# Optimization experiments

Hardware: AMD Instinct MI355X
Metric: run time of the kernel (lower is better)

## Reference

```python
import jax, jax.numpy as jnp
import numpy as np

TIMESTEPS = 1000
ZERO_W = 1.0
NONZERO_W = 1.0
VT_W = 1.0
VX_W = 1.0
VY_W = 1.0


def _holographic_transform(x, timesteps, transpose):
    """x: (B,1,H,W) -> (B,1,H,timesteps).
    For each nonzero pixel (h,w) with value v, write w (the column index) at
    time bin q = int(v*timesteps)-1 (negative q wraps, as torch's x[-1]=...).
    Torch iterates nonzeros in row-major order so on collisions the largest
    column index wins -> scatter-max reproduces that deterministically.
    """
    img = x[:, 0]
    if transpose:  # virtual_dim == 'x'
        img = jnp.swapaxes(img, 1, 2)
    B, H, W = img.shape
    q = (img * timesteps).astype(jnp.int32) - 1
    # zeros -> out-of-range index `timesteps`, dropped by mode='drop';
    # nonzeros: wrap -1 -> timesteps-1 like torch negative indexing
    q = jnp.where(img != 0, q % timesteps, timesteps)
    ycoord = jnp.broadcast_to(jnp.arange(W, dtype=x.dtype), (B, H, W))
    b_idx = jnp.arange(B)[:, None, None]
    h_idx = jnp.arange(H)[None, :, None]
    out = jnp.zeros((B, H, timesteps), x.dtype)
    out = out.at[b_idx, h_idx, q].max(ycoord, mode='drop')
    return out[:, None]


def _acb_mse(recon, target, zero_w, nonzero_w):
    zero_mask = target == 0
    d2 = (recon - target) ** 2
    c0 = zero_mask.sum()
    c1 = (~zero_mask).sum()
    # mean over each class; empty class (NaN in torch) -> 0
    l0 = jnp.where(c0 > 0, jnp.where(zero_mask, d2, 0.0).sum() / jnp.maximum(c0, 1), 0.0)
    l1 = jnp.where(c1 > 0, jnp.where(zero_mask, 0.0, d2).sum() / jnp.maximum(c1, 1), 0.0)
    return zero_w * l0 + nonzero_w * l1


def setup_inputs() -> dict:
    key = jax.random.key(0)
    k1, k2, k3, k4 = jax.random.split(key, 4)
    B, H, W = 32, 512, 512

    def sparse_img(kv, km):
        v = jax.random.uniform(kv, (B, 1, H, W), dtype=jnp.float32)
        keep = jax.random.uniform(km, (B, 1, H, W)) < 0.05
        return jnp.where(keep, v, 0.0)

    return {
        "reconstructed_image": sparse_img(k1, k2),
        "target_image": sparse_img(k3, k4),
    }


def reference(reconstructed_image, target_image):
    vt = _acb_mse(reconstructed_image, target_image, ZERO_W, NONZERO_W) * VT_W

    rx = _holographic_transform(reconstructed_image, TIMESTEPS, transpose=True)
    tx = _holographic_transform(target_image, TIMESTEPS, transpose=True)
    vx = _acb_mse(rx, tx, ZERO_W, NONZERO_W) * VX_W

    ry = _holographic_transform(reconstructed_image, TIMESTEPS, transpose=False)
    ty = _holographic_transform(target_image, TIMESTEPS, transpose=False)
    vy = _acb_mse(ry, ty, ZERO_W, NONZERO_W) * VY_W

    return vt + vx + vy
```

## Files before the change

kernel.cpp:

```cpp
#include <hip/hip_runtime.h>

#define TS 1000

__device__ __forceinline__ double wred(double v) {
#pragma unroll
    for (int o = 32; o > 0; o >>= 1) v += __shfl_down(v, o, 64);
    return v;
}

__device__ __forceinline__ void scat(unsigned* bins, float v, unsigned val) {
    if (v != 0.0f) {
        int q = (int)(v * 1000.0f) - 1;
        if (q < 0) q += TS;
        atomicMax(&bins[q], val);
    }
}

__global__ void kinit(double* acc, int n) {
    int i = blockIdx.x * blockDim.x + threadIdx.x;
    if (i < n) acc[i] = 0.0;
}

__global__ __launch_bounds__(256, 4) void kmain(const float* __restrict__ R,
                                                const float* __restrict__ T,
                                                double* __restrict__ acc,
                                                int ncopy_mask) {
    __shared__ unsigned bins[8000];
    const int tid = threadIdx.x;
    const uint4 z4 = make_uint4(0u, 0u, 0u, 0u);

    {
        uint4* p = (uint4*)bins;
        for (int i = tid; i < 2000; i += 256) p[i] = z4;
    }
    __syncthreads();

    const int lane = tid & 63, wv = tid >> 6;
    const int id = blockIdx.x;
    double* accrow = acc + (size_t)(id & ncopy_mask) * 16;

    double s0 = 0.0, ssum = 0.0;
    int c1 = 0;

    if ((id & 1) == 0) {
        const int kid = id >> 1;
        double t0 = 0.0, tsum = 0.0;
        int tc1 = 0;
        unsigned* bR = bins + wv * 2000;
        unsigned* bT = bR + 1000;
        uint4* r4 = (uint4*)bR;
        uint4* t4 = (uint4*)bT;
        for (int it = 0; it < 4; it++) {
            const size_t row = (size_t)kid * 16 + (size_t)(wv * 4 + it);
            const float4* R4 = (const float4*)(R + row * 512);
            const float4* T4 = (const float4*)(T + row * 512);
#pragma unroll
            for (int k = 0; k < 2; k++) {
                const int c = lane + k * 64;
                float4 rv = R4[c];
                float4 tv = T4[c];
                float rr[4] = {rv.x, rv.y, rv.z, rv.w};
                float tt[4] = {tv.x, tv.y, tv.z, tv.w};
#pragma unroll
                for (int j = 0; j < 4; j++) {
                    float a = rr[j], b = tt[j];
                    float d = a - b, d2 = d * d;
                    bool bz = (b == 0.0f);
                    tsum += (double)d2;
                    t0 += bz ? (double)d2 : 0.0;
                    tc1 += bz ? 0 : 1;
                    scat(bR, a, (unsigned)(c * 4 + j));
                    scat(bT, b, (unsigned)(c * 4 + j));
                }
            }
            __syncthreads();
            for (int g = lane; g < 250; g += 64) {
                uint4 rg = r4[g], tg = t4[g];
                if (rg.x | rg.y | rg.z | rg.w | tg.x | tg.y | tg.z | tg.w) {
                    r4[g] = z4;
                    t4[g] = z4;
                    unsigned ru[4] = {rg.x, rg.y, rg.z, rg.w};
                    unsigned tu[4] = {tg.x, tg.y, tg.z, tg.w};
#pragma unroll
                    for (int j2 = 0; j2 < 4; j2++) {
                        float rb = (float)ru[j2], tb = (float)tu[j2];
                        float d = rb - tb, d2 = d * d;
                        bool tz = (tb == 0.0f);
                        ssum += (double)d2;
                        s0 += tz ? (double)d2 : 0.0;
                        c1 += tz ? 0 : 1;
                    }
                }
            }
            __syncthreads();
        }
        double v0 = wred(t0), v1 = wred(tsum), v2 = wred((double)tc1);
        double v3 = wred(s0), v4 = wred(ssum), v5 = wred((double)c1);
        if (lane == 0) {
            atomicAdd(&accrow[0], v0);
            atomicAdd(&accrow[1], v1);
            atomicAdd(&accrow[2], v2);
            atomicAdd(&accrow[3], v3);
            atomicAdd(&accrow[4], v4);
            atomicAdd(&accrow[5], v5);
        }
    } else {
        const int kid = id >> 1;
        const int b = kid >> 5;
        const int line = kid & 31;
        const float* Rb = R + (size_t)b * (512 * 512) + (size_t)line * 16;
        const float* Tb = T + (size_t)b * (512 * 512) + (size_t)line * 16;

        float4 ra[8], ta[8];
#pragma unroll
        for (int k = 0; k < 8; k++) {
            const int h = k * 64 + (tid >> 2);
            const int sub = (tid + k) & 3;
            const size_t off = (size_t)h * 512 + sub * 4;
            ra[k] = *(const float4*)(Rb + off);
            ta[k] = *(const float4*)(Tb + off);
        }

        uint4* r4 = (uint4*)bins;
        uint4* t4 = (uint4*)(bins + 4000);
#pragma unroll
        for (int p = 0; p < 4; p++) {
#pragma unroll
            for (int k = 0; k < 8; k++) {
                if (((tid + k) & 3) == p) {
                    const unsigned h = (unsigned)(k * 64 + (tid >> 2));
                    scat(bins + 0 * 1000, ra[k].x, h);
                    scat(bins + 1 * 1000, ra[k].y, h);
                    scat(bins + 2 * 1000, ra[k].z, h);
                    scat(bins + 3 * 1000, ra[k].w, h);
                    scat(bins + 4000 + 0 * 1000, ta[k].x, h);
                    scat(bins + 4000 + 1 * 1000, ta[k].y, h);
                    scat(bins + 4000 + 2 * 1000, ta[k].z, h);
                    scat(bins + 4000 + 3 * 1000, ta[k].w, h);
                }
            }
            __syncthreads();
            for (int g = tid; g < 1000; g += 256) {
                uint4 rg = r4[g], tg = t4[g];
                if (rg.x | rg.y | rg.z | rg.w | tg.x | tg.y | tg.z | tg.w) {
                    r4[g] = z4;
                    t4[g] = z4;
                    unsigned ru[4] = {rg.x, rg.y, rg.z, rg.w};
                    unsigned tu[4] = {tg.x, tg.y, tg.z, tg.w};
#pragma unroll
                    for (int j = 0; j < 4; j++) {
                        float rb = (float)ru[j], tb = (float)tu[j];
                        float d = rb - tb, d2 = d * d;
                        bool tz = (tb == 0.0f);
                        ssum += (double)d2;
                        s0 += tz ? (double)d2 : 0.0;
                        c1 += tz ? 0 : 1;
                    }
                }
            }
            __syncthreads();
        }
        double v3 = wred(s0), v4 = wred(ssum), v5 = wred((double)c1);
        if (lane == 0) {
            atomicAdd(&accrow[6], v3);
            atomicAdd(&accrow[7], v4);
            atomicAdd(&accrow[8], v5);
        }
    }
}

__global__ void kfin(const double* __restrict__ acc, float* __restrict__ out,
                     int ncopy) {
    const int lane = threadIdx.x;
    double v[9];
#pragma unroll
    for (int k = 0; k < 9; k++) v[k] = 0.0;
    if (lane < ncopy) {
#pragma unroll
        for (int k = 0; k < 9; k++) v[k] = acc[(size_t)lane * 16 + k];
    }
#pragma unroll
    for (int k = 0; k < 9; k++) {
#pragma unroll
        for (int o = 16; o > 0; o >>= 1) v[k] += __shfl_down(v[k], o, 64);
    }
    if (lane == 0) {
        const double NT = 8388608.0;
        const double NB = 16384000.0;
        double vt_c1 = v[2], vy_c1 = v[5], vx_c1 = v[8];
        double vt_c0 = NT - vt_c1, vy_c0 = NB - vy_c1, vx_c0 = NB - vx_c1;
        double vt_s1 = v[1] - v[0];
        double vy_s1 = v[4] - v[3];
        double vx_s1 = v[7] - v[6];
        double vt = (vt_c0 > 0.0 ? v[0] / vt_c0 : 0.0) +
                    (vt_c1 > 0.0 ? vt_s1 / vt_c1 : 0.0);
        double vy = (vy_c0 > 0.0 ? v[3] / vy_c0 : 0.0) +
                    (vy_c1 > 0.0 ? vy_s1 / vy_c1 : 0.0);
        double vx = (vx_c0 > 0.0 ? v[6] / vx_c0 : 0.0) +
                    (vx_c1 > 0.0 ? vx_s1 / vx_c1 : 0.0);
        out[0] = (float)(vt + vx + vy);
    }
}

extern "C" void kernel_launch(void* const* d_in, const int* in_sizes, int n_in,
                              void* d_out, int out_size, void* d_ws, size_t ws_size,
                              hipStream_t stream) {
    const float* R = (const float*)d_in[0];
    const float* T = (const float*)d_in[1];
    double* acc = (double*)d_ws;
    float* out = (float*)d_out;

    int ncopy = 16;
    while (ncopy > 1 && (size_t)ncopy * 16 * sizeof(double) > ws_size) ncopy >>= 1;

    hipLaunchKernelGGL(kinit, dim3(1), dim3(256), 0, stream, acc, ncopy * 16);
    hipLaunchKernelGGL(kmain, dim3(2048), dim3(256), 0, stream, R, T, acc, ncopy - 1);
    hipLaunchKernelGGL(kfin, dim3(1), dim3(64), 0, stream, acc, out, ncopy);
}
```

Baseline: 83.10 us.

## Fuse finalize into main kernel, use float accumulators, raise occupancy bound

Drops the separate init and finalize kernels. A memset now clears the workspace, and a last-block-done atomic counter lets the final block compute the loss inside the main kernel. Per-thread accumulators switch from double to float and are widened to double only for the warp reduction. The launch bound moves from 4 to 5 blocks per CU, and one trailing barrier is removed. The float accumulation slightly reduces precision, and the fused finalize adds a threadfence plus an atomic counter per block.

Result: slower. 146.7 us (+76.5%).

```diff
diff --git a/kernel.cpp b/kernel.cpp
--- a/kernel.cpp
+++ b/kernel.cpp
@@ -16,15 +16,12 @@
     }
 }
 
-__global__ void kinit(double* acc, int n) {
-    int i = blockIdx.x * blockDim.x + threadIdx.x;
-    if (i < n) acc[i] = 0.0;
-}
-
-__global__ __launch_bounds__(256, 4) void kmain(const float* __restrict__ R,
+__global__ __launch_bounds__(256, 5) void kmain(const float* __restrict__ R,
                                                 const float* __restrict__ T,
                                                 double* __restrict__ acc,
-                                                int ncopy_mask) {
+                                                int ncopy_mask, int ncopy,
+                                                unsigned* __restrict__ done,
+                                                float* __restrict__ out) {
     __shared__ unsigned bins[8000];
     const int tid = threadIdx.x;
     const uint4 z4 = make_uint4(0u, 0u, 0u, 0u);
@@ -39,12 +36,12 @@
     const int id = blockIdx.x;
     double* accrow = acc + (size_t)(id & ncopy_mask) * 16;
 
-    double s0 = 0.0, ssum = 0.0;
+    float s0 = 0.0f, ssum = 0.0f;
     int c1 = 0;
 
     if ((id & 1) == 0) {
         const int kid = id >> 1;
-        double t0 = 0.0, tsum = 0.0;
+        float t0 = 0.0f, tsum = 0.0f;
         int tc1 = 0;
         unsigned* bR = bins + wv * 2000;
         unsigned* bT = bR + 1000;
@@ -66,8 +63,8 @@
                     float a = rr[j], b = tt[j];
                     float d = a - b, d2 = d * d;
                     bool bz = (b == 0.0f);
-                    tsum += (double)d2;
-                    t0 += bz ? (double)d2 : 0.0;
+                    tsum += d2;
+                    t0 += bz ? d2 : 0.0f;
                     tc1 += bz ? 0 : 1;
                     scat(bR, a, (unsigned)(c * 4 + j));
                     scat(bT, b, (unsigned)(c * 4 + j));
@@ -86,16 +83,16 @@
                         float rb = (float)ru[j2], tb = (float)tu[j2];
                         float d = rb - tb, d2 = d * d;
                         bool tz = (tb == 0.0f);
-                        ssum += (double)d2;
-                        s0 += tz ? (double)d2 : 0.0;
+                        ssum += d2;
+                        s0 += tz ? d2 : 0.0f;
                         c1 += tz ? 0 : 1;
                     }
                 }
             }
             __syncthreads();
         }
-        double v0 = wred(t0), v1 = wred(tsum), v2 = wred((double)tc1);
-        double v3 = wred(s0), v4 = wred(ssum), v5 = wred((double)c1);
+        double v0 = wred((double)t0), v1 = wred((double)tsum), v2 = wred((double)tc1);
+        double v3 = wred((double)s0), v4 = wred((double)ssum), v5 = wred((double)c1);
         if (lane == 0) {
             atomicAdd(&accrow[0], v0);
             atomicAdd(&accrow[1], v1);
@@ -152,53 +149,50 @@
                         float rb = (float)ru[j], tb = (float)tu[j];
                         float d = rb - tb, d2 = d * d;
                         bool tz = (tb == 0.0f);
-                        ssum += (double)d2;
-                        s0 += tz ? (double)d2 : 0.0;
+                        ssum += d2;
+                        s0 += tz ? d2 : 0.0f;
                         c1 += tz ? 0 : 1;
                     }
                 }
             }
-            __syncthreads();
-        }
-        double v3 = wred(s0), v4 = wred(ssum), v5 = wred((double)c1);
+            if (p < 3) __syncthreads();
+        }
+        double v3 = wred((double)s0), v4 = wred((double)ssum), v5 = wred((double)c1);
         if (lane == 0) {
             atomicAdd(&accrow[6], v3);
             atomicAdd(&accrow[7], v4);
             atomicAdd(&accrow[8], v5);
         }
     }
-}
-
-__global__ void kfin(const double* __restrict__ acc, float* __restrict__ out,
-                     int ncopy) {
-    const int lane = threadIdx.x;
-    double v[9];
-#pragma unroll
-    for (int k = 0; k < 9; k++) v[k] = 0.0;
-    if (lane < ncopy) {
-#pragma unroll
-        for (int k = 0; k < 9; k++) v[k] = acc[(size_t)lane * 16 + k];
-    }
-#pragma unroll
-    for (int k = 0; k < 9; k++) {
-#pragma unroll
-        for (int o = 16; o > 0; o >>= 1) v[k] += __shfl_down(v[k], o, 64);
-    }
-    if (lane == 0) {
-        const double NT = 8388608.0;
-        const double NB = 16384000.0;
-        double vt_c1 = v[2], vy_c1 = v[5], vx_c1 = v[8];
-        double vt_c0 = NT - vt_c1, vy_c0 = NB - vy_c1, vx_c0 = NB - vx_c1;
-        double vt_s1 = v[1] - v[0];
-        double vy_s1 = v[4] - v[3];
-        double vx_s1 = v[7] - v[6];
-        double vt = (vt_c0 > 0.0 ? v[0] / vt_c0 : 0.0) +
-                    (vt_c1 > 0.0 ? vt_s1 / vt_c1 : 0.0);
-        double vy = (vy_c0 > 0.0 ? v[3] / vy_c0 : 0.0) +
-                    (vy_c1 > 0.0 ? vy_s1 / vy_c1 : 0.0);
-        double vx = (vx_c0 > 0.0 ? v[6] / vx_c0 : 0.0) +
-                    (vx_c1 > 0.0 ? vx_s1 / vx_c1 : 0.0);
-        out[0] = (float)(vt + vx + vy);
+
+    __syncthreads();
+    if (tid == 0) {
+        __threadfence();
+        if (atomicAdd(done, 1u) == (unsigned)(gridDim.x - 1)) {
+            __threadfence();
+            double v[9];
+#pragma unroll
+            for (int k = 0; k < 9; k++) v[k] = 0.0;
+            for (int i = 0; i < ncopy; i++) {
+#pragma unroll
+                for (int k = 0; k < 9; k++)
+                    v[k] += atomicAdd(&acc[(size_t)i * 16 + k], 0.0);
+            }
+            const double NT = 8388608.0;
+            const double NB = 16384000.0;
+            double vt_c1 = v[2], vy_c1 = v[5], vx_c1 = v[8];
+            double vt_c0 = NT - vt_c1, vy_c0 = NB - vy_c1, vx_c0 = NB - vx_c1;
+            double vt_s1 = v[1] - v[0];
+            double vy_s1 = v[4] - v[3];
+            double vx_s1 = v[7] - v[6];
+            double vt = (vt_c0 > 0.0 ? v[0] / vt_c0 : 0.0) +
+                        (vt_c1 > 0.0 ? vt_s1 / vt_c1 : 0.0);
+            double vy = (vy_c0 > 0.0 ? v[3] / vy_c0 : 0.0) +
+                        (vy_c1 > 0.0 ? vy_s1 / vy_c1 : 0.0);
+            double vx = (vx_c0 > 0.0 ? v[6] / vx_c0 : 0.0) +
+                        (vx_c1 > 0.0 ? vx_s1 / vx_c1 : 0.0);
+            out[0] = (float)(vt + vx + vy);
+        }
     }
 }
 
@@ -211,9 +205,13 @@
     float* out = (float*)d_out;
 
     int ncopy = 16;
-    while (ncopy > 1 && (size_t)ncopy * 16 * sizeof(double) > ws_size) ncopy >>= 1;
-
-    hipLaunchKernelGGL(kinit, dim3(1), dim3(256), 0, stream, acc, ncopy * 16);
-    hipLaunchKernelGGL(kmain, dim3(2048), dim3(256), 0, stream, R, T, acc, ncopy - 1);
-    hipLaunchKernelGGL(kfin, dim3(1), dim3(64), 0, stream, acc, out, ncopy);
-}
+    while (ncopy > 1 &&
+           (size_t)ncopy * 16 * sizeof(double) + sizeof(unsigned) > ws_size)
+        ncopy >>= 1;
+    unsigned* done = (unsigned*)(acc + (size_t)ncopy * 16);
+
+    hipMemsetAsync(d_ws, 0, (size_t)ncopy * 16 * sizeof(double) + sizeof(unsigned),
+                   stream);
+    hipLaunchKernelGGL(kmain, dim3(2048), dim3(256), 0, stream, R, T, acc,
+                       ncopy - 1, ncopy, done, out);
+}
```

## Use persistent blocks with atomic ticket work queue and float accumulators

Applied to the files above, without the earlier changes.

Replaces the fixed one-unit-per-block grid with 1280 persistent blocks that pull work units (1024 column units first, then 4096 row units of four rows each) from a global atomic ticket counter. Row units now cover four rows per block instead of sixteen, and the per-wave row path drops its block-wide barriers. Per-thread accumulators switch from double to float and are reduced once per block at the end. The aim is better load balance, fewer block launches, fewer atomics and cheaper FP64 adds. The cost is a per-unit global atomic plus barrier, and some risk of float rounding error in the sums.

Result: slower. 137.2 us (+65.1%).

```diff
diff --git a/kernel.cpp b/kernel.cpp
--- a/kernel.cpp
+++ b/kernel.cpp
@@ -1,6 +1,9 @@
 #include <hip/hip_runtime.h>
 
 #define TS 1000
+#define NCOL 1024u
+#define NROWU 4096u
+#define NUNITS (NCOL + NROWU)
 
 __device__ __forceinline__ double wred(double v) {
 #pragma unroll
@@ -16,42 +19,99 @@
     }
 }
 
-__global__ void kinit(double* acc, int n) {
+__global__ void kinit(unsigned* w, int n) {
     int i = blockIdx.x * blockDim.x + threadIdx.x;
-    if (i < n) acc[i] = 0.0;
+    if (i < n) w[i] = 0u;
 }
 
 __global__ __launch_bounds__(256, 4) void kmain(const float* __restrict__ R,
                                                 const float* __restrict__ T,
                                                 double* __restrict__ acc,
-                                                int ncopy_mask) {
+                                                int ncopy_mask,
+                                                unsigned* __restrict__ ticket) {
     __shared__ unsigned bins[8000];
+    __shared__ unsigned u_sh;
     const int tid = threadIdx.x;
+    const int lane = tid & 63, wv = tid >> 6;
     const uint4 z4 = make_uint4(0u, 0u, 0u, 0u);
+    double* accrow = acc + (size_t)(blockIdx.x & ncopy_mask) * 16;
 
     {
         uint4* p = (uint4*)bins;
         for (int i = tid; i < 2000; i += 256) p[i] = z4;
     }
-    __syncthreads();
-
-    const int lane = tid & 63, wv = tid >> 6;
-    const int id = blockIdx.x;
-    double* accrow = acc + (size_t)(id & ncopy_mask) * 16;
-
-    double s0 = 0.0, ssum = 0.0;
-    int c1 = 0;
-
-    if ((id & 1) == 0) {
-        const int kid = id >> 1;
-        double t0 = 0.0, tsum = 0.0;
-        int tc1 = 0;
-        unsigned* bR = bins + wv * 2000;
-        unsigned* bT = bR + 1000;
-        uint4* r4 = (uint4*)bR;
-        uint4* t4 = (uint4*)bT;
-        for (int it = 0; it < 4; it++) {
-            const size_t row = (size_t)kid * 16 + (size_t)(wv * 4 + it);
+
+    float t0 = 0.f, tsum = 0.f;  int tc1 = 0;
+    float ys0 = 0.f, yss = 0.f;  int yc1 = 0;
+    float xs0 = 0.f, xss = 0.f;  int xc1 = 0;
+
+    unsigned* bR = bins + wv * 2000;
+    unsigned* bT = bR + 1000;
+    uint4* r4w = (uint4*)bR;
+    uint4* t4w = (uint4*)bT;
+    uint4* r4b = (uint4*)bins;
+    uint4* t4b = (uint4*)(bins + 4000);
+
+    for (;;) {
+        if (tid == 0) u_sh = atomicAdd(ticket, 1u);
+        __syncthreads();
+        const unsigned u = u_sh;
+        if (u >= NUNITS) break;
+
+        if (u < NCOL) {
+            const int b = (int)(u >> 5);
+            const int line = (int)(u & 31u);
+            const float* Rb = R + (size_t)b * (512 * 512) + (size_t)line * 16;
+            const float* Tb = T + (size_t)b * (512 * 512) + (size_t)line * 16;
+
+            float4 ra[8], ta[8];
+#pragma unroll
+            for (int k = 0; k < 8; k++) {
+                const int h = k * 64 + (tid >> 2);
+                const int sub = (tid + k) & 3;
+                const size_t off = (size_t)h * 512 + sub * 4;
+                ra[k] = *(const float4*)(Rb + off);
+                ta[k] = *(const float4*)(Tb + off);
+            }
+#pragma unroll
+            for (int p = 0; p < 4; p++) {
+#pragma unroll
+                for (int k = 0; k < 8; k++) {
+                    if (((tid + k) & 3) == p) {
+                        const unsigned h = (unsigned)(k * 64 + (tid >> 2));
+                        scat(bins + 0 * 1000, ra[k].x, h);
+                        scat(bins + 1 * 1000, ra[k].y, h);
+                        scat(bins + 2 * 1000, ra[k].z, h);
+                        scat(bins + 3 * 1000, ra[k].w, h);
+                        scat(bins + 4000 + 0 * 1000, ta[k].x, h);
+                        scat(bins + 4000 + 1 * 1000, ta[k].y, h);
+                        scat(bins + 4000 + 2 * 1000, ta[k].z, h);
+                        scat(bins + 4000 + 3 * 1000, ta[k].w, h);
+                    }
+                }
+                __syncthreads();
+                for (int g = tid; g < 1000; g += 256) {
+                    uint4 rg = r4b[g], tg = t4b[g];
+                    if (rg.x | rg.y | rg.z | rg.w | tg.x | tg.y | tg.z | tg.w) {
+                        r4b[g] = z4;
+                        t4b[g] = z4;
+                        unsigned ru[4] = {rg.x, rg.y, rg.z, rg.w};
+                        unsigned tu[4] = {tg.x, tg.y, tg.z, tg.w};
+#pragma unroll
+                        for (int j = 0; j < 4; j++) {
+                            float rb = (float)ru[j], tb = (float)tu[j];
+                            float d = rb - tb, d2 = d * d;
+                            bool tz = (tb == 0.0f);
+                            xss += d2;
+                            xs0 += tz ? d2 : 0.0f;
+                            xc1 += tz ? 0 : 1;
+                        }
+                    }
+                }
+                if (p < 3) __syncthreads();
+            }
+        } else {
+            const size_t row = (size_t)(u - NCOL) * 4 + (size_t)wv;
             const float4* R4 = (const float4*)(R + row * 512);
             const float4* T4 = (const float4*)(T + row * 512);
 #pragma unroll
@@ -66,19 +126,18 @@
                     float a = rr[j], b = tt[j];
                     float d = a - b, d2 = d * d;
                     bool bz = (b == 0.0f);
-                    tsum += (double)d2;
-                    t0 += bz ? (double)d2 : 0.0;
+                    tsum += d2;
+                    t0 += bz ? d2 : 0.0f;
                     tc1 += bz ? 0 : 1;
                     scat(bR, a, (unsigned)(c * 4 + j));
                     scat(bT, b, (unsigned)(c * 4 + j));
                 }
             }
-            __syncthreads();
             for (int g = lane; g < 250; g += 64) {
-                uint4 rg = r4[g], tg = t4[g];
+                uint4 rg = r4w[g], tg = t4w[g];
                 if (rg.x | rg.y | rg.z | rg.w | tg.x | tg.y | tg.z | tg.w) {
-                    r4[g] = z4;
-                    t4[g] = z4;
+                    r4w[g] = z4;
+                    t4w[g] = z4;
                     unsigned ru[4] = {rg.x, rg.y, rg.z, rg.w};
                     unsigned tu[4] = {tg.x, tg.y, tg.z, tg.w};
 #pragma unroll
@@ -86,86 +145,29 @@
                         float rb = (float)ru[j2], tb = (float)tu[j2];
                         float d = rb - tb, d2 = d * d;
                         bool tz = (tb == 0.0f);
-                        ssum += (double)d2;
-                        s0 += tz ? (double)d2 : 0.0;
-                        c1 += tz ? 0 : 1;
+                        yss += d2;
+                        ys0 += tz ? d2 : 0.0f;
+                        yc1 += tz ? 0 : 1;
                     }
                 }
             }
-            __syncthreads();
         }
-        double v0 = wred(t0), v1 = wred(tsum), v2 = wred((double)tc1);
-        double v3 = wred(s0), v4 = wred(ssum), v5 = wred((double)c1);
-        if (lane == 0) {
-            atomicAdd(&accrow[0], v0);
-            atomicAdd(&accrow[1], v1);
-            atomicAdd(&accrow[2], v2);
-            atomicAdd(&accrow[3], v3);
-            atomicAdd(&accrow[4], v4);
-            atomicAdd(&accrow[5], v5);
-        }
-    } else {
-        const int kid = id >> 1;
-        const int b = kid >> 5;
-        const int line = kid & 31;
-        const float* Rb = R + (size_t)b * (512 * 512) + (size_t)line * 16;
-        const float* Tb = T + (size_t)b * (512 * 512) + (size_t)line * 16;
-
-        float4 ra[8], ta[8];
-#pragma unroll
-        for (int k = 0; k < 8; k++) {
-            const int h = k * 64 + (tid >> 2);
-            const int sub = (tid + k) & 3;
-            const size_t off = (size_t)h * 512 + sub * 4;
-            ra[k] = *(const float4*)(Rb + off);
-            ta[k] = *(const float4*)(Tb + off);
-        }
-
-        uint4* r4 = (uint4*)bins;
-        uint4* t4 = (uint4*)(bins + 4000);
-#pragma unroll
-        for (int p = 0; p < 4; p++) {
-#pragma unroll
-            for (int k = 0; k < 8; k++) {
-                if (((tid + k) & 3) == p) {
-                    const unsigned h = (unsigned)(k * 64 + (tid >> 2));
-                    scat(bins + 0 * 1000, ra[k].x, h);
-                    scat(bins + 1 * 1000, ra[k].y, h);
-                    scat(bins + 2 * 1000, ra[k].z, h);
-                    scat(bins + 3 * 1000, ra[k].w, h);
-                    scat(bins + 4000 + 0 * 1000, ta[k].x, h);
-                    scat(bins + 4000 + 1 * 1000, ta[k].y, h);
-                    scat(bins + 4000 + 2 * 1000, ta[k].z, h);
-                    scat(bins + 4000 + 3 * 1000, ta[k].w, h);
-                }
-            }
-            __syncthreads();
-            for (int g = tid; g < 1000; g += 256) {
-                uint4 rg = r4[g], tg = t4[g];
-                if (rg.x | rg.y | rg.z | rg.w | tg.x | tg.y | tg.z | tg.w) {
-                    r4[g] = z4;
-                    t4[g] = z4;
-                    unsigned ru[4] = {rg.x, rg.y, rg.z, rg.w};
-                    unsigned tu[4] = {tg.x, tg.y, tg.z, tg.w};
-#pragma unroll
-                    for (int j = 0; j < 4; j++) {
-                        float rb = (float)ru[j], tb = (float)tu[j];
-                        float d = rb - tb, d2 = d * d;
-                        bool tz = (tb == 0.0f);
-                        ssum += (double)d2;
-                        s0 += tz ? (double)d2 : 0.0;
-                        c1 += tz ? 0 : 1;
-                    }
-                }
-            }
-            __syncthreads();
-        }
-        double v3 = wred(s0), v4 = wred(ssum), v5 = wred((double)c1);
-        if (lane == 0) {
-            atomicAdd(&accrow[6], v3);
-            atomicAdd(&accrow[7], v4);
-            atomicAdd(&accrow[8], v5);
-        }
+        __syncthreads();
+    }
+
+    double v0 = wred((double)t0), v1 = wred((double)tsum), v2 = wred((double)tc1);
+    double v3 = wred((double)ys0), v4 = wred((double)yss), v5 = wred((double)yc1);
+    double v6 = wred((double)xs0), v7 = wred((double)xss), v8 = wred((double)xc1);
+    if (lane == 0) {
+        atomicAdd(&accrow[0], v0);
+        atomicAdd(&accrow[1], v1);
+        atomicAdd(&accrow[2], v2);
+        atomicAdd(&accrow[3], v3);
+        atomicAdd(&accrow[4], v4);
+        atomicAdd(&accrow[5], v5);
+        atomicAdd(&accrow[6], v6);
+        atomicAdd(&accrow[7], v7);
+        atomicAdd(&accrow[8], v8);
     }
 }
 
@@ -211,9 +213,14 @@
     float* out = (float*)d_out;
 
     int ncopy = 16;
-    while (ncopy > 1 && (size_t)ncopy * 16 * sizeof(double) > ws_size) ncopy >>= 1;
-
-    hipLaunchKernelGGL(kinit, dim3(1), dim3(256), 0, stream, acc, ncopy * 16);
-    hipLaunchKernelGGL(kmain, dim3(2048), dim3(256), 0, stream, R, T, acc, ncopy - 1);
+    while (ncopy > 1 &&
+           (size_t)ncopy * 16 * sizeof(double) + sizeof(unsigned) > ws_size)
+        ncopy >>= 1;
+    unsigned* ticket = (unsigned*)(acc + (size_t)ncopy * 16);
+
+    hipLaunchKernelGGL(kinit, dim3(4), dim3(256), 0, stream,
+                       (unsigned*)d_ws, ncopy * 32 + 1);
+    hipLaunchKernelGGL(kmain, dim3(1280), dim3(256), 0, stream, R, T, acc,
+                       ncopy - 1, ticket);
     hipLaunchKernelGGL(kfin, dim3(1), dim3(64), 0, stream, acc, out, ncopy);
 }
```
